# Performance work log

Measured on AMD Instinct MI355X. Metric: run time of the kernel, lower is better.

## Reference

```python
import jax, jax.numpy as jnp
import numpy as np

B, T, D, H, DK, DV = 2, 2048, 1024, 16, 64, 64
_MASK_ADDER = -10000.0  # tf-models MaskedSoftmax convention


def setup_inputs() -> dict:
    key = jax.random.key(0)
    ks = jax.random.split(key, 8)
    s = 0.02
    return {
        "query": jax.random.normal(ks[0], (B, T, D), jnp.float32),
        "value": jax.random.normal(ks[1], (B, T, D), jnp.float32),
        "Wq": jax.random.normal(ks[2], (D, H, DK), jnp.float32) * s,
        "bq": jnp.zeros((H, DK), jnp.float32),
        "Wk": jax.random.normal(ks[3], (D, H, DK), jnp.float32) * s,
        "bk": jnp.zeros((H, DK), jnp.float32),
        "Wv": jax.random.normal(ks[4], (D, H, DV), jnp.float32) * s,
        "bv": jnp.zeros((H, DV), jnp.float32),
        "Wo": jax.random.normal(ks[5], (H, DV, D), jnp.float32) * s,
        "bo": jnp.zeros((D,), jnp.float32),
        "attention_mask": jnp.ones((B, T, T), jnp.int32),
    }


def reference(query, value, Wq, bq, Wk, bk, Wv, bv, Wo, bo, attention_mask):
    # key defaults to value (call() with key=None); training=False -> no dropout
    q = jnp.einsum("btd,dhk->bthk", query, Wq) + bq          # [B,T,H,DK]
    k = jnp.einsum("bsd,dhk->bshk", value, Wk) + bk          # [B,S,H,DK]
    v = jnp.einsum("bsd,dhk->bshk", value, Wv) + bv          # [B,S,H,DV]
    q = q * (1.0 / jnp.sqrt(jnp.asarray(DK, q.dtype)))
    scores = jnp.einsum("bthk,bshk->bhts", q, k)             # [B,H,T,S]
    # MaskedSoftmax: expand mask at axis 1, additive -10000 on masked slots
    adder = (1.0 - attention_mask.astype(scores.dtype))[:, None, :, :] * _MASK_ADDER
    probs = jax.nn.softmax(scores + adder, axis=-1)
    ctx = jnp.einsum("bhts,bshv->bthv", probs, v)            # [B,T,H,DV]
    out = jnp.einsum("bthv,hvd->btd", ctx, Wo) + bo          # [B,T,D]
    return out
```

## Files before the change

### kernel.cpp

```cpp
#include <hip/hip_runtime.h>
#include <hip/hip_bf16.h>
#include <stdint.h>

#define TSEQ 2048
#define DMODEL 1024
#define NHEAD 16
#define HDIM 64
#define MROWS 4096
#define L2E 1.44269504088896340736f

typedef unsigned short u16;
typedef unsigned int u32;
typedef __attribute__((ext_vector_type(8))) short bf16x8;
typedef __attribute__((ext_vector_type(8))) unsigned short u16x8;
typedef __attribute__((ext_vector_type(4))) unsigned short u16x4;
typedef __attribute__((ext_vector_type(4))) float f32x4;
typedef __attribute__((ext_vector_type(16))) float f32x16;
typedef __attribute__((ext_vector_type(4))) unsigned int u32x4;

__device__ inline u16 f2bf(float f) {
  __hip_bfloat16 h(f);
  return __builtin_bit_cast(u16, h);
}

__device__ inline float fexp2(float x) { float r; asm("v_exp_f32 %0, %1" : "=v"(r) : "v"(x)); return r; }

__device__ inline unsigned cvtpk_bf16(float a, float b) {
  unsigned r; asm("v_cvt_pk_bf16_f32 %0, %1, %2" : "=v"(r) : "v"(a), "v"(b)); return r;
}

__device__ inline void permswap(u32& a, u32& b) {
  asm volatile("v_permlane32_swap_b32 %0, %1" : "+v"(a), "+v"(b));
}

__device__ inline void gload16(const void* g, void* l) {
  __builtin_amdgcn_global_load_lds((const __attribute__((address_space(1))) void*)g,
                                   (__attribute__((address_space(3))) void*)l, 16, 0, 0);
}

__global__ void cvt2(const float* __restrict__ q, const float* __restrict__ v,
                     u16* __restrict__ qo, u16* __restrict__ vo) {
  const float* in = blockIdx.y ? v : q;
  u16* out = blockIdx.y ? vo : qo;
  int i = (blockIdx.x * blockDim.x + threadIdx.x) * 4;
  float4 x = *(const float4*)(in + i);
  u16x4 o;
  o.x = f2bf(x.x); o.y = f2bf(x.y); o.z = f2bf(x.z); o.w = f2bf(x.w);
  *(u16x4*)(out + i) = o;
}

__global__ void wtrans4(const float* __restrict__ Wq, const float* __restrict__ Wk,
                        const float* __restrict__ Wv, const float* __restrict__ Wo,
                        u16* __restrict__ WT3, u16* __restrict__ WoT) {
  __shared__ float tile[32][33];
  const int z = blockIdx.z;
  const float* W = z == 0 ? Wq : z == 1 ? Wk : z == 2 ? Wv : Wo;
  u16* WT = z < 3 ? (WT3 + (size_t)z * 1024 * 1024) : WoT;
  const int bx = blockIdx.x, by = blockIdx.y;
  const int tr = threadIdx.x >> 3;
  const int tc4 = (threadIdx.x & 7) * 4;
  float4 v = *(const float4*)(W + (size_t)(by * 32 + tr) * 1024 + bx * 32 + tc4);
  tile[tr][tc4 + 0] = v.x; tile[tr][tc4 + 1] = v.y;
  tile[tr][tc4 + 2] = v.z; tile[tr][tc4 + 3] = v.w;
  __syncthreads();
  u16x4 o;
  o.x = f2bf(tile[tc4 + 0][tr]); o.y = f2bf(tile[tc4 + 1][tr]);
  o.z = f2bf(tile[tc4 + 2][tr]); o.w = f2bf(tile[tc4 + 3][tr]);
  *(u16x4*)(WT + (size_t)(bx * 32 + tr) * 1024 + by * 32 + tc4) = o;
}

__global__ void maskflag(const int* __restrict__ mask, int* __restrict__ flags) {
  const int st = blockIdx.x, qt = blockIdx.y, b = blockIdx.z;
  const int row = qt * 128 + (threadIdx.x >> 1);
  const int col0 = st * 128 + (threadIdx.x & 1) * 64;
  const int* p = mask + (size_t)b * TSEQ * TSEQ + (size_t)row * TSEQ + col0;
  int ok = 1;
  #pragma unroll
  for (int j = 0; j < 64; j += 4) {
    int4 v = *(const int4*)(p + j);
    ok &= (v.x == 1) & (v.y == 1) & (v.z == 1) & (v.w == 1);
  }
  ok = __all(ok);
  __shared__ int s[4];
  if ((threadIdx.x & 63) == 0) s[threadIdx.x >> 6] = ok;
  __syncthreads();
  if (threadIdx.x == 0) flags[(b * 16 + qt) * 16 + st] = s[0] & s[1] & s[2] & s[3];
}

__global__ void vtrans(const u16* __restrict__ V, u16* __restrict__ VT) {
  __shared__ u16 tile[64][72];
  const int bh = blockIdx.y;
  const int t0 = blockIdx.x * 64;
  const u16* src = V + ((size_t)bh * TSEQ + t0) * 64;
  const int r = threadIdx.x >> 3, sg = threadIdx.x & 7;
  #pragma unroll
  for (int i = 0; i < 2; ++i) {
    int row = r + i * 32;
    u16x8 v = *(const u16x8*)(src + (size_t)row * 64 + sg * 8);
    #pragma unroll
    for (int j = 0; j < 8; ++j) tile[row][sg * 8 + j] = v[j];
  }
  __syncthreads();
  u16* dst = VT + (size_t)bh * 64 * TSEQ;
  #pragma unroll
  for (int i = 0; i < 2; ++i) {
    int v = r + i * 32;
    u16x8 o;
    #pragma unroll
    for (int j = 0; j < 8; ++j) o[j] = tile[sg * 8 + j][v];
    *(u16x8*)(dst + (size_t)v * TSEQ + t0 + sg * 8) = o;
  }
}

__global__ __launch_bounds__(256) void gemm_qkv(
    const u16* __restrict__ qxb, const u16* __restrict__ vxb, const u16* __restrict__ WT3,
    const float* __restrict__ bq, const float* __restrict__ bk, const float* __restrict__ bv,
    u16* __restrict__ Qb, u16* __restrict__ Kb, u16* __restrict__ Vb, float qscale) {
  __shared__ u16 As[128 * 64];
  __shared__ u16 Bs[128 * 64];
  const int tid = threadIdx.x;
  const int w = tid >> 6, lane = tid & 63;
  const int lo = lane & 15, hi = lane >> 4;
  const int m0 = blockIdx.x * 128, n0 = blockIdx.y * 128;
  const int nsel = n0 >> 10;
  const u16* A = nsel == 0 ? qxb : vxb;
  const float* bias = nsel == 0 ? bq : nsel == 1 ? bk : bv;
  u16* dst = nsel == 0 ? Qb : nsel == 1 ? Kb : Vb;
  const float scl = nsel == 0 ? qscale : 1.0f;
  const int wm = (w >> 1) * 64, wn = (w & 1) * 64;
  f32x4 acc[4][4] = {};
  const int loff = w * 4096 + lane * 16;
  for (int kt = 0; kt < 16; ++kt) {
    #pragma unroll
    for (int i = 0; i < 4; ++i) {
      const int off = loff + i * 1024;
      const int row = off >> 7;
      const int g = ((off >> 4) & 7) ^ (row & 7);
      gload16(A + (size_t)(m0 + row) * 1024 + kt * 64 + g * 8, (char*)As + off);
      gload16(WT3 + (size_t)(n0 + row) * 1024 + kt * 64 + g * 8, (char*)Bs + off);
    }
    __syncthreads();
    #pragma unroll
    for (int kk = 0; kk < 2; ++kk) {
      bf16x8 af[4], bfr[4];
      #pragma unroll
      for (int mi = 0; mi < 4; ++mi) {
        int row = wm + mi * 16 + lo;
        af[mi] = *(const bf16x8*)(As + row * 64 + (((kk * 4 + hi) ^ (row & 7)) << 3));
      }
      #pragma unroll
      for (int ni = 0; ni < 4; ++ni) {
        int row = wn + ni * 16 + lo;
        bfr[ni] = *(const bf16x8*)(Bs + row * 64 + (((kk * 4 + hi) ^ (row & 7)) << 3));
      }
      #pragma unroll
      for (int mi = 0; mi < 4; ++mi)
        #pragma unroll
        for (int ni = 0; ni < 4; ++ni)
          acc[mi][ni] = __builtin_amdgcn_mfma_f32_16x16x32_bf16(af[mi], bfr[ni], acc[mi][ni], 0, 0, 0);
    }
    __syncthreads();
  }
  #pragma unroll
  for (int ni = 0; ni < 4; ++ni) {
    const int col = (n0 + wn + ni * 16 + lo) & 1023;
    const float bc = bias[col];
    #pragma unroll
    for (int mi = 0; mi < 4; ++mi) {
      #pragma unroll
      for (int r = 0; r < 4; ++r) {
        const int row = m0 + wm + mi * 16 + hi * 4 + r;
        const float v = (acc[mi][ni][r] + bc) * scl;
        dst[(size_t)(((row >> 11) * NHEAD + (col >> 6)) * TSEQ + (row & 2047)) * HDIM + (col & 63)] = f2bf(v);
      }
    }
  }
}

__global__ __launch_bounds__(256) void gemm_o(const u16* __restrict__ A, const u16* __restrict__ BT,
                                              const float* __restrict__ bias, float* __restrict__ C) {
  __shared__ u16 As[64 * 64];
  __shared__ u16 Bs[128 * 64];
  const int tid = threadIdx.x;
  const int w = tid >> 6, lane = tid & 63;
  const int lo = lane & 15, hi = lane >> 4;
  const int m0 = blockIdx.x * 64, n0 = blockIdx.y * 128;
  const int wm = (w >> 1) * 32, wn = (w & 1) * 64;
  f32x4 acc[2][4] = {};
  for (int kt = 0; kt < 16; ++kt) {
    #pragma unroll
    for (int i = 0; i < 2; ++i) {
      const int off = tid * 16 + i * 4096;
      const int row = off >> 7;
      const int g = ((off >> 4) & 7) ^ (row & 7);
      gload16(A + (size_t)(m0 + row) * 1024 + kt * 64 + g * 8, (char*)As + off);
    }
    #pragma unroll
    for (int i = 0; i < 4; ++i) {
      const int off = tid * 16 + i * 4096;
      const int row = off >> 7;
      const int g = ((off >> 4) & 7) ^ (row & 7);
      gload16(BT + (size_t)(n0 + row) * 1024 + kt * 64 + g * 8, (char*)Bs + off);
    }
    __syncthreads();
    #pragma unroll
    for (int kk = 0; kk < 2; ++kk) {
      bf16x8 af[2], bfr[4];
      #pragma unroll
      for (int mi = 0; mi < 2; ++mi) {
        int row = wm + mi * 16 + lo;
        af[mi] = *(const bf16x8*)(As + row * 64 + (((kk * 4 + hi) ^ (row & 7)) << 3));
      }
      #pragma unroll
      for (int ni = 0; ni < 4; ++ni) {
        int row = wn + ni * 16 + lo;
        bfr[ni] = *(const bf16x8*)(Bs + row * 64 + (((kk * 4 + hi) ^ (row & 7)) << 3));
      }
      #pragma unroll
      for (int mi = 0; mi < 2; ++mi)
        #pragma unroll
        for (int ni = 0; ni < 4; ++ni)
          acc[mi][ni] = __builtin_amdgcn_mfma_f32_16x16x32_bf16(af[mi], bfr[ni], acc[mi][ni], 0, 0, 0);
    }
    __syncthreads();
  }
  #pragma unroll
  for (int ni = 0; ni < 4; ++ni) {
    const int col = n0 + wn + ni * 16 + lo;
    const float bc = bias[col];
    #pragma unroll
    for (int mi = 0; mi < 2; ++mi)
      #pragma unroll
      for (int r = 0; r < 4; ++r) {
        const int row = m0 + wm + mi * 16 + hi * 4 + r;
        C[(size_t)row * DMODEL + col] = acc[mi][ni][r] + bc;
      }
  }
}

__global__ __launch_bounds__(256) void flash(
    const u16* __restrict__ Q, const u16* __restrict__ K, const u16* __restrict__ VT,
    const int* __restrict__ mask, const int* __restrict__ flags, u16* __restrict__ ctx) {
  __shared__ u16 Ks[2][64 * 64];
  __shared__ u16 Vs[2][64 * 64];
  const int tid = threadIdx.x, w = tid >> 6, lane = tid & 63;
  const int l5 = lane & 31, hi2 = lane >> 5;
  const int qt = blockIdx.x, bh = blockIdx.y;
  const int b = bh >> 4, h = bh & 15;
  const int tq = qt * 128 + w * 32;

  const int soff = w * 2048 + lane * 16;
  const int srow0 = w * 16 + (lane >> 3);
  const int g8 = (((lane & 7) ^ (lane >> 3)) << 3);

  bf16x8 qf[4];
  #pragma unroll
  for (int kc = 0; kc < 4; ++kc)
    qf[kc] = *(const bf16x8*)(Q + ((size_t)bh * TSEQ + tq + l5) * 64 + kc * 16 + hi2 * 8);

  unsigned fl = 0;
  {
    const int* fp = flags + (b * 16 + qt) * 16;
    #pragma unroll
    for (int i = 0; i < 4; ++i) {
      int4 v = *(const int4*)(fp + i * 4);
      fl |= (unsigned)((v.x & 1) | ((v.y & 1) << 1) | ((v.z & 1) << 2) | ((v.w & 1) << 3)) << (4 * i);
    }
  }

  f32x16 o0 = {}, o1 = {};
  float mrow = -1e30f, lrow = 0.f;

#define STAGE(buf, st_) do {                                                         \
    const u16* kb_ = K + ((size_t)bh * TSEQ + (st_) * 64) * 64;                      \
    const u16* vb_ = VT + (size_t)bh * 64 * TSEQ + (st_) * 64;                       \
    gload16(kb_ + (size_t)srow0 * 64 + g8, (char*)Ks[buf] + soff);                   \
    gload16(kb_ + (size_t)(srow0 + 8) * 64 + g8, (char*)Ks[buf] + soff + 1024);      \
    gload16(vb_ + (size_t)srow0 * TSEQ + g8, (char*)Vs[buf] + soff);                 \
    gload16(vb_ + (size_t)(srow0 + 8) * TSEQ + g8, (char*)Vs[buf] + soff + 1024);    \
  } while (0)

  int cur = 0;
  STAGE(0, 0);
  __syncthreads();

  for (int st = 0; st < 32; ++st) {
    if (st < 31) STAGE(cur ^ 1, st + 1);
    const u16* Ksb = Ks[cur];
    const u16* Vsb = Vs[cur];

    f32x16 s0 = {}, s1 = {};
    __builtin_amdgcn_s_setprio(1);
    #pragma unroll
    for (int kc = 0; kc < 4; ++kc) {
      const int sg = kc * 2 + hi2;
      {
        const int row = l5;
        bf16x8 kf = *(const bf16x8*)(Ksb + row * 64 + ((sg ^ (row & 7)) << 3));
        s0 = __builtin_amdgcn_mfma_f32_32x32x16_bf16(kf, qf[kc], s0, 0, 0, 0);
      }
      {
        const int row = 32 + l5;
        bf16x8 kf = *(const bf16x8*)(Ksb + row * 64 + ((sg ^ (row & 7)) << 3));
        s1 = __builtin_amdgcn_mfma_f32_32x32x16_bf16(kf, qf[kc], s1, 0, 0, 0);
      }
    }
    __builtin_amdgcn_s_setprio(0);

    if (!((fl >> (st >> 1)) & 1)) {
      const int t = tq + l5;
      const int* mrowp = mask + ((size_t)b * TSEQ + t) * TSEQ + st * 64;
      #pragma unroll
      for (int r = 0; r < 16; ++r) {
        const int sr = (r & 3) + 8 * (r >> 2) + 4 * hi2;
        s0[r] += (1.0f - (float)mrowp[sr]) * -14426.950408f;
        s1[r] += (1.0f - (float)mrowp[sr + 32]) * -14426.950408f;
      }
    }

    float pm;
    {
      f32x16 m01;
      #pragma unroll
      for (int r = 0; r < 16; ++r) m01[r] = fmaxf(s0[r], s1[r]);
      #pragma unroll
      for (int half = 8; half >= 1; half >>= 1)
        #pragma unroll
        for (int r = 0; r < 8; ++r)
          if (r < half) m01[r] = fmaxf(m01[r], m01[r + half]);
      pm = fmaxf(m01[0], __shfl_xor(m01[0], 32));
    }

    if (__any(pm - mrow > 11.0f)) {
      const float mn = fmaxf(mrow, pm);
      const float a = fexp2(mrow - mn);
      lrow *= a;
      mrow = mn;
      #pragma unroll
      for (int r = 0; r < 16; ++r) {
        const float ar = __shfl(a, (r & 3) + 8 * (r >> 2) + 4 * hi2);
        o0[r] *= ar;
        o1[r] *= ar;
      }
    }

    float rs = 0.f;
    u32 W0[8], W1[8];
    #pragma unroll
    for (int q = 0; q < 4; ++q)
      #pragma unroll
      for (int c = 0; c < 2; ++c) {
        const int r = 4 * q + 2 * c;
        float a0 = fexp2(s0[r] - mrow), b0 = fexp2(s0[r + 1] - mrow);
        float a1 = fexp2(s1[r] - mrow), b1 = fexp2(s1[r + 1] - mrow);
        rs += (a0 + b0) + (a1 + b1);
        W0[q * 2 + c] = cvtpk_bf16(a0, b0);
        W1[q * 2 + c] = cvtpk_bf16(a1, b1);
      }
    rs += __shfl_xor(rs, 32);
    lrow += rs;

    bf16x8 pa[4];
    #pragma unroll
    for (int ts = 0; ts < 2; ++ts)
      #pragma unroll
      for (int qp = 0; qp < 2; ++qp) {
        u32 d0 = ts ? W1[(2 * qp) * 2 + 0] : W0[(2 * qp) * 2 + 0];
        u32 e0 = ts ? W1[(2 * qp + 1) * 2 + 0] : W0[(2 * qp + 1) * 2 + 0];
        u32 d1 = ts ? W1[(2 * qp) * 2 + 1] : W0[(2 * qp) * 2 + 1];
        u32 e1 = ts ? W1[(2 * qp + 1) * 2 + 1] : W0[(2 * qp + 1) * 2 + 1];
        permswap(d0, e0);
        permswap(d1, e1);
        u32x4 fw;
        fw.x = d0; fw.y = d1; fw.z = e0; fw.w = e1;
        pa[ts * 2 + qp] = __builtin_bit_cast(bf16x8, fw);
      }

    __builtin_amdgcn_s_setprio(1);
    #pragma unroll
    for (int kc2 = 0; kc2 < 4; ++kc2) {
      const int sg = kc2 * 2 + hi2;
      {
        const int row = l5;
        bf16x8 vf = *(const bf16x8*)(Vsb + row * 64 + ((sg ^ (row & 7)) << 3));
        o0 = __builtin_amdgcn_mfma_f32_32x32x16_bf16(pa[kc2], vf, o0, 0, 0, 0);
      }
      {
        const int row = 32 + l5;
        bf16x8 vf = *(const bf16x8*)(Vsb + row * 64 + ((sg ^ (row & 7)) << 3));
        o1 = __builtin_amdgcn_mfma_f32_32x32x16_bf16(pa[kc2], vf, o1, 0, 0, 0);
      }
    }
    __builtin_amdgcn_s_setprio(0);

    __syncthreads();
    cur ^= 1;
  }
#undef STAGE

  const float inv = 1.0f / lrow;
  #pragma unroll
  for (int r = 0; r < 16; ++r) {
    const int sr = (r & 3) + 8 * (r >> 2) + 4 * hi2;
    const float ir = __shfl(inv, sr);
    u16* cp = ctx + (size_t)(b * TSEQ + tq + sr) * DMODEL + h * 64;
    cp[l5] = f2bf(o0[r] * ir);
    cp[32 + l5] = f2bf(o1[r] * ir);
  }
}

extern "C" void kernel_launch(void* const* d_in, const int* in_sizes, int n_in,
                              void* d_out, int out_size, void* d_ws, size_t ws_size,
                              hipStream_t stream) {
  (void)in_sizes; (void)n_in; (void)out_size; (void)ws_size;
  const float* query = (const float*)d_in[0];
  const float* value = (const float*)d_in[1];
  const float* Wq = (const float*)d_in[2];
  const float* bq = (const float*)d_in[3];
  const float* Wk = (const float*)d_in[4];
  const float* bk = (const float*)d_in[5];
  const float* Wv = (const float*)d_in[6];
  const float* bv = (const float*)d_in[7];
  const float* Wo = (const float*)d_in[8];
  const float* bo = (const float*)d_in[9];
  const int* amask = (const int*)d_in[10];

  char* ws = (char*)d_ws;
  const size_t MB = 1 << 20;
  u16* qxb = (u16*)(ws + 0 * MB);
  u16* vxb = (u16*)(ws + 8 * MB);
  u16* WT3 = (u16*)(ws + 16 * MB);
  u16* WoT = (u16*)(ws + 22 * MB);
  u16* Qb  = (u16*)(ws + 24 * MB);
  u16* Kb  = (u16*)(ws + 32 * MB);
  u16* Vb  = (u16*)(ws + 40 * MB);
  u16* VTb = (u16*)(ws + 48 * MB);
  u16* ctx = (u16*)(ws + 56 * MB);
  int* flg = (int*)(ws + 64 * MB);

  cvt2<<<dim3(4096, 2), 256, 0, stream>>>(query, value, qxb, vxb);
  wtrans4<<<dim3(32, 32, 4), 256, 0, stream>>>(Wq, Wk, Wv, Wo, WT3, WoT);
  maskflag<<<dim3(16, 16, 2), 256, 0, stream>>>(amask, flg);

  gemm_qkv<<<dim3(32, 24), 256, 0, stream>>>(qxb, vxb, WT3, bq, bk, bv, Qb, Kb, Vb, 0.125f * L2E);
  vtrans<<<dim3(32, 32), 256, 0, stream>>>(Vb, VTb);
  flash<<<dim3(16, 32), 256, 0, stream>>>(Qb, Kb, VTb, amask, flg, ctx);
  gemm_o<<<dim3(64, 8), 256, 0, stream>>>(ctx, WoT, bo, (float*)d_out);
}
```

Baseline: 150.3 us.

## Software-pipeline flash loop: overlap PV of previous tile with QK of current

Restructures the attention inner loop so the P·V MFMAs for tile t-1 are issued alongside the Q·K MFMAs for tile t, with the softmax for tile t following. V gets a triple-buffered LDS ring and P fragments are ping-ponged between two register sets. The LDS swizzle also gains an extra XOR term on row>>3 to cut bank conflicts. The aim is to hide softmax latency behind matrix work, at the cost of more LDS and more live registers, which may reduce occupancy.

```diff
diff --git a/kernel.cpp b/kernel.cpp
--- a/kernel.cpp
+++ b/kernel.cpp
@@ -242,7 +242,7 @@
     const u16* __restrict__ Q, const u16* __restrict__ K, const u16* __restrict__ VT,
     const int* __restrict__ mask, const int* __restrict__ flags, u16* __restrict__ ctx) {
   __shared__ u16 Ks[2][64 * 64];
-  __shared__ u16 Vs[2][64 * 64];
+  __shared__ u16 Vs[3][64 * 64];
   const int tid = threadIdx.x, w = tid >> 6, lane = tid & 63;
   const int l5 = lane & 31, hi2 = lane >> 5;
   const int qt = blockIdx.x, bh = blockIdx.y;
@@ -251,7 +251,8 @@
 
   const int soff = w * 2048 + lane * 16;
   const int srow0 = w * 16 + (lane >> 3);
-  const int g8 = (((lane & 7) ^ (lane >> 3)) << 3);
+  const int lg0 = (((lane & 7) ^ (lane >> 3) ^ ((w * 2) & 3)) << 3);
+  const int lg1 = (((lane & 7) ^ (lane >> 3) ^ ((w * 2 + 1) & 3)) << 3);
 
   bf16x8 qf[4];
   #pragma unroll
@@ -270,133 +271,127 @@
 
   f32x16 o0 = {}, o1 = {};
   float mrow = -1e30f, lrow = 0.f;
-
-#define STAGE(buf, st_) do {                                                         \
-    const u16* kb_ = K + ((size_t)bh * TSEQ + (st_) * 64) * 64;                      \
-    const u16* vb_ = VT + (size_t)bh * 64 * TSEQ + (st_) * 64;                       \
-    gload16(kb_ + (size_t)srow0 * 64 + g8, (char*)Ks[buf] + soff);                   \
-    gload16(kb_ + (size_t)(srow0 + 8) * 64 + g8, (char*)Ks[buf] + soff + 1024);      \
-    gload16(vb_ + (size_t)srow0 * TSEQ + g8, (char*)Vs[buf] + soff);                 \
-    gload16(vb_ + (size_t)(srow0 + 8) * TSEQ + g8, (char*)Vs[buf] + soff + 1024);    \
+  bf16x8 paA[4], paB[4];
+
+#define STAGE_K(buf, st_) do {                                                        \
+    const u16* kb_ = K + ((size_t)bh * TSEQ + (st_) * 64) * 64;                       \
+    gload16(kb_ + (size_t)srow0 * 64 + lg0, (char*)Ks[buf] + soff);                   \
+    gload16(kb_ + (size_t)(srow0 + 8) * 64 + lg1, (char*)Ks[buf] + soff + 1024);      \
   } while (0)
-
-  int cur = 0;
-  STAGE(0, 0);
+#define STAGE_V(buf, st_) do {                                                        \
+    const u16* vb_ = VT + (size_t)bh * 64 * TSEQ + (st_) * 64;                        \
+    gload16(vb_ + (size_t)srow0 * TSEQ + lg0, (char*)Vs[buf] + soff);                 \
+    gload16(vb_ + (size_t)(srow0 + 8) * TSEQ + lg1, (char*)Vs[buf] + soff + 1024);    \
+  } while (0)
+
+#define FR(base, row, sg) \
+  (*(const bf16x8*)((base) + (row) * 64 + ((((sg) ^ ((row) & 7) ^ (((row) >> 3) & 3)) << 3))))
+
+#define QKC(T, S0, S1) do {                                                           \
+    const u16* Kb_ = Ks[(T) & 1];                                                     \
+    _Pragma("unroll") for (int kc = 0; kc < 4; ++kc) {                                \
+      const int sg = kc * 2 + hi2;                                                    \
+      S0 = __builtin_amdgcn_mfma_f32_32x32x16_bf16(FR(Kb_, l5, sg), qf[kc], S0, 0, 0, 0); \
+      S1 = __builtin_amdgcn_mfma_f32_32x32x16_bf16(FR(Kb_, 32 + l5, sg), qf[kc], S1, 0, 0, 0); \
+    } } while (0)
+
+#define PVC(VB, PA) do {                                                              \
+    const u16* Vb_ = Vs[VB];                                                          \
+    _Pragma("unroll") for (int kc = 0; kc < 4; ++kc) {                                \
+      const int sg = kc * 2 + hi2;                                                    \
+      o0 = __builtin_amdgcn_mfma_f32_32x32x16_bf16(PA[kc], FR(Vb_, l5, sg), o0, 0, 0, 0); \
+      o1 = __builtin_amdgcn_mfma_f32_32x32x16_bf16(PA[kc], FR(Vb_, 32 + l5, sg), o1, 0, 0, 0); \
+    } } while (0)
+
+#define SMAX(T, S0, S1, PAOUT) do {                                                   \
+    if (!((fl >> ((T) >> 1)) & 1)) {                                                  \
+      const int t_ = tq + l5;                                                         \
+      const int* mp_ = mask + ((size_t)b * TSEQ + t_) * TSEQ + (T) * 64;              \
+      _Pragma("unroll") for (int r = 0; r < 16; ++r) {                                \
+        const int sr_ = (r & 3) + 8 * (r >> 2) + 4 * hi2;                             \
+        S0[r] += (1.0f - (float)mp_[sr_]) * -14426.950408f;                           \
+        S1[r] += (1.0f - (float)mp_[sr_ + 32]) * -14426.950408f;                      \
+      } }                                                                             \
+    float c0 = fmaxf(S0[0], S1[0]), c1 = fmaxf(S0[1], S1[1]);                         \
+    float c2 = fmaxf(S0[2], S1[2]), c3 = fmaxf(S0[3], S1[3]);                         \
+    _Pragma("unroll") for (int r = 4; r < 16; r += 4) {                               \
+      c0 = fmaxf(c0, fmaxf(S0[r], S1[r]));     c1 = fmaxf(c1, fmaxf(S0[r+1], S1[r+1])); \
+      c2 = fmaxf(c2, fmaxf(S0[r+2], S1[r+2])); c3 = fmaxf(c3, fmaxf(S0[r+3], S1[r+3])); } \
+    float pm = fmaxf(fmaxf(c0, c1), fmaxf(c2, c3));                                   \
+    pm = fmaxf(pm, __shfl_xor(pm, 32));                                               \
+    if (__any(pm - mrow > 11.0f)) {                                                   \
+      const float mn_ = fmaxf(mrow, pm);                                              \
+      const float a_ = fexp2(mrow - mn_);                                             \
+      lrow *= a_; mrow = mn_;                                                         \
+      _Pragma("unroll") for (int r = 0; r < 16; ++r) {                                \
+        const float ar_ = __shfl(a_, (r & 3) + 8 * (r >> 2) + 4 * hi2);               \
+        o0[r] *= ar_; o1[r] *= ar_; } }                                               \
+    float rs = 0.f; u32 W0_[8], W1_[8];                                               \
+    _Pragma("unroll") for (int q_ = 0; q_ < 4; ++q_)                                  \
+      _Pragma("unroll") for (int c_ = 0; c_ < 2; ++c_) {                              \
+        const int r = 4 * q_ + 2 * c_;                                                \
+        float a0 = fexp2(S0[r] - mrow), b0 = fexp2(S0[r + 1] - mrow);                 \
+        float a1 = fexp2(S1[r] - mrow), b1 = fexp2(S1[r + 1] - mrow);                 \
+        rs += (a0 + b0) + (a1 + b1);                                                  \
+        W0_[q_ * 2 + c_] = cvtpk_bf16(a0, b0);                                        \
+        W1_[q_ * 2 + c_] = cvtpk_bf16(a1, b1); }                                      \
+    rs += __shfl_xor(rs, 32); lrow += rs;                                             \
+    _Pragma("unroll") for (int ts = 0; ts < 2; ++ts)                                  \
+      _Pragma("unroll") for (int qp = 0; qp < 2; ++qp) {                              \
+        u32 d0 = ts ? W1_[(2 * qp) * 2 + 0] : W0_[(2 * qp) * 2 + 0];                  \
+        u32 e0 = ts ? W1_[(2 * qp + 1) * 2 + 0] : W0_[(2 * qp + 1) * 2 + 0];          \
+        u32 d1 = ts ? W1_[(2 * qp) * 2 + 1] : W0_[(2 * qp) * 2 + 1];                  \
+        u32 e1 = ts ? W1_[(2 * qp + 1) * 2 + 1] : W0_[(2 * qp + 1) * 2 + 1];          \
+        permswap(d0, e0); permswap(d1, e1);                                           \
+        u32x4 fw_; fw_.x = d0; fw_.y = d1; fw_.z = e0; fw_.w = e1;                    \
+        PAOUT[ts * 2 + qp] = __builtin_bit_cast(bf16x8, fw_); }                       \
+  } while (0)
+
+#define BODY(T, VPREV, VNEXT, DOSTAGE, PAIN, PAOUT) do {                              \
+    if (DOSTAGE) { STAGE_K(((T) + 1) & 1, (T) + 1); STAGE_V(VNEXT, (T) + 1); }        \
+    f32x16 s0 = {}, s1 = {};                                                          \
+    __builtin_amdgcn_s_setprio(1);                                                    \
+    QKC(T, s0, s1);                                                                   \
+    PVC(VPREV, PAIN);                                                                 \
+    __builtin_amdgcn_s_setprio(0);                                                    \
+    SMAX(T, s0, s1, PAOUT);                                                           \
+    __syncthreads();                                                                  \
+  } while (0)
+
+  STAGE_K(0, 0); STAGE_V(0, 0);
   __syncthreads();
-
-  for (int st = 0; st < 32; ++st) {
-    if (st < 31) STAGE(cur ^ 1, st + 1);
-    const u16* Ksb = Ks[cur];
-    const u16* Vsb = Vs[cur];
-
+  {
     f32x16 s0 = {}, s1 = {};
     __builtin_amdgcn_s_setprio(1);
-    #pragma unroll
-    for (int kc = 0; kc < 4; ++kc) {
-      const int sg = kc * 2 + hi2;
-      {
-        const int row = l5;
-        bf16x8 kf = *(const bf16x8*)(Ksb + row * 64 + ((sg ^ (row & 7)) << 3));
-        s0 = __builtin_amdgcn_mfma_f32_32x32x16_bf16(kf, qf[kc], s0, 0, 0, 0);
-      }
-      {
-        const int row = 32 + l5;
-        bf16x8 kf = *(const bf16x8*)(Ksb + row * 64 + ((sg ^ (row & 7)) << 3));
-        s1 = __builtin_amdgcn_mfma_f32_32x32x16_bf16(kf, qf[kc], s1, 0, 0, 0);
-      }
-    }
+    QKC(0, s0, s1);
     __builtin_amdgcn_s_setprio(0);
-
-    if (!((fl >> (st >> 1)) & 1)) {
-      const int t = tq + l5;
-      const int* mrowp = mask + ((size_t)b * TSEQ + t) * TSEQ + st * 64;
-      #pragma unroll
-      for (int r = 0; r < 16; ++r) {
-        const int sr = (r & 3) + 8 * (r >> 2) + 4 * hi2;
-        s0[r] += (1.0f - (float)mrowp[sr]) * -14426.950408f;
-        s1[r] += (1.0f - (float)mrowp[sr + 32]) * -14426.950408f;
-      }
-    }
-
-    float pm;
-    {
-      f32x16 m01;
-      #pragma unroll
-      for (int r = 0; r < 16; ++r) m01[r] = fmaxf(s0[r], s1[r]);
-      #pragma unroll
-      for (int half = 8; half >= 1; half >>= 1)
-        #pragma unroll
-        for (int r = 0; r < 8; ++r)
-          if (r < half) m01[r] = fmaxf(m01[r], m01[r + half]);
-      pm = fmaxf(m01[0], __shfl_xor(m01[0], 32));
-    }
-
-    if (__any(pm - mrow > 11.0f)) {
-      const float mn = fmaxf(mrow, pm);
-      const float a = fexp2(mrow - mn);
-      lrow *= a;
-      mrow = mn;
-      #pragma unroll
-      for (int r = 0; r < 16; ++r) {
-        const float ar = __shfl(a, (r & 3) + 8 * (r >> 2) + 4 * hi2);
-        o0[r] *= ar;
-        o1[r] *= ar;
-      }
-    }
-
-    float rs = 0.f;
-    u32 W0[8], W1[8];
-    #pragma unroll
-    for (int q = 0; q < 4; ++q)
-      #pragma unroll
-      for (int c = 0; c < 2; ++c) {
-        const int r = 4 * q + 2 * c;
-        float a0 = fexp2(s0[r] - mrow), b0 = fexp2(s0[r + 1] - mrow);
-        float a1 = fexp2(s1[r] - mrow), b1 = fexp2(s1[r + 1] - mrow);
-        rs += (a0 + b0) + (a1 + b1);
-        W0[q * 2 + c] = cvtpk_bf16(a0, b0);
-        W1[q * 2 + c] = cvtpk_bf16(a1, b1);
-      }
-    rs += __shfl_xor(rs, 32);
-    lrow += rs;
-
-    bf16x8 pa[4];
-    #pragma unroll
-    for (int ts = 0; ts < 2; ++ts)
-      #pragma unroll
-      for (int qp = 0; qp < 2; ++qp) {
-        u32 d0 = ts ? W1[(2 * qp) * 2 + 0] : W0[(2 * qp) * 2 + 0];
-        u32 e0 = ts ? W1[(2 * qp + 1) * 2 + 0] : W0[(2 * qp + 1) * 2 + 0];
-        u32 d1 = ts ? W1[(2 * qp) * 2 + 1] : W0[(2 * qp) * 2 + 1];
-        u32 e1 = ts ? W1[(2 * qp + 1) * 2 + 1] : W0[(2 * qp + 1) * 2 + 1];
-        permswap(d0, e0);
-        permswap(d1, e1);
-        u32x4 fw;
-        fw.x = d0; fw.y = d1; fw.z = e0; fw.w = e1;
-        pa[ts * 2 + qp] = __builtin_bit_cast(bf16x8, fw);
-      }
-
-    __builtin_amdgcn_s_setprio(1);
-    #pragma unroll
-    for (int kc2 = 0; kc2 < 4; ++kc2) {
-      const int sg = kc2 * 2 + hi2;
-      {
-        const int row = l5;
-        bf16x8 vf = *(const bf16x8*)(Vsb + row * 64 + ((sg ^ (row & 7)) << 3));
-        o0 = __builtin_amdgcn_mfma_f32_32x32x16_bf16(pa[kc2], vf, o0, 0, 0, 0);
-      }
-      {
-        const int row = 32 + l5;
-        bf16x8 vf = *(const bf16x8*)(Vsb + row * 64 + ((sg ^ (row & 7)) << 3));
-        o1 = __builtin_amdgcn_mfma_f32_32x32x16_bf16(pa[kc2], vf, o1, 0, 0, 0);
-      }
-    }
-    __builtin_amdgcn_s_setprio(0);
-
+    STAGE_K(1, 1); STAGE_V(1, 1);
+    SMAX(0, s0, s1, paA);
     __syncthreads();
-    cur ^= 1;
-  }
-#undef STAGE
+  }
+
+  int vp = 0, vn = 2;
+  for (int t = 1; t < 31; t += 2) {
+    BODY(t, vp, vn, 1, paA, paB);
+    const int vp2 = (vp + 1 == 3) ? 0 : vp + 1;
+    const int vn2 = (vn + 1 == 3) ? 0 : vn + 1;
+    BODY(t + 1, vp2, vn2, 1, paB, paA);
+    vp = (vp2 + 1 == 3) ? 0 : vp2 + 1;
+    vn = (vn2 + 1 == 3) ? 0 : vn2 + 1;
+  }
+  BODY(31, vp, 0, 0, paA, paB);
+
+  __builtin_amdgcn_s_setprio(1);
+  PVC(1, paB);
+  __builtin_amdgcn_s_setprio(0);
+
+#undef BODY
+#undef SMAX
+#undef PVC
+#undef QKC
+#undef FR
+#undef STAGE_V
+#undef STAGE_K
 
   const float inv = 1.0f / lrow;
   #pragma unroll
```

Result: faster. 144.7 us (-3.7%).
